# Performance work log

Hardware: AMD Instinct MI355X
Metric: run time of the kernel (lower is better)

Reference implementation:

```python
import jax, jax.numpy as jnp
import numpy as np

N, E = 100000, 1600000
IN_C, H, C = 256, 4, 64
NEG_SLOPE = 0.2


def setup_inputs() -> dict:
    key = jax.random.key(0)
    k1, k2, k3, k4, k5 = jax.random.split(key, 5)
    x = jax.random.normal(k1, (N, IN_C), dtype=jnp.float32)
    edge_index = jax.random.randint(k2, (2, E), 0, N, dtype=jnp.int64)
    # GATConv params: lin weight [IN_C, H*C], attention vectors [H, C], bias [C] (concat=False)
    W = jax.random.normal(k3, (IN_C, H * C), dtype=jnp.float32) / np.sqrt(IN_C)
    att_src = jax.random.normal(k4, (H, C), dtype=jnp.float32) / np.sqrt(C)
    att_dst = jax.random.normal(k5, (H, C), dtype=jnp.float32) / np.sqrt(C)
    bias = jnp.zeros((C,), dtype=jnp.float32)
    return {"x": x, "edge_index": edge_index, "W": W,
            "att_src": att_src, "att_dst": att_dst, "bias": bias}


def reference(x, edge_index, W, att_src, att_dst, bias):
    n = x.shape[0]
    # GATConv adds self-loops by default
    loops = jnp.arange(n, dtype=edge_index.dtype)
    src = jnp.concatenate([edge_index[0], loops])  # message source j
    dst = jnp.concatenate([edge_index[1], loops])  # message target i

    h = (x @ W).reshape(n, H, C)                       # [N,H,C]
    a_src = jnp.einsum('nhc,hc->nh', h, att_src)       # [N,H]
    a_dst = jnp.einsum('nhc,hc->nh', h, att_dst)       # [N,H]

    e = jax.nn.leaky_relu(a_src[src] + a_dst[dst], NEG_SLOPE)  # [E+N,H]
    m = jax.ops.segment_max(e, dst, num_segments=n)            # per-target max
    e = jnp.exp(e - m[dst])
    denom = jax.ops.segment_sum(e, dst, num_segments=n)
    alpha = e / (denom[dst] + 1e-16)                           # softmax over incoming edges

    out = jax.ops.segment_sum(alpha[:, :, None] * h[src], dst, num_segments=n)  # [N,H,C]
    return out.mean(axis=1) + bias  # concat=False -> mean over heads, [N,C]
```

## Files before the change

### kernel.cpp

```cpp
#include <hip/hip_runtime.h>

#define N_NODES 100000
#define N_EDGES 1600000
#define TOT (N_EDGES + N_NODES)
#define IN_CH 256
#define NHEAD 4
#define CH 64
#define HC 256
#define NEG_SLOPE 0.2f

typedef _Float16 half8 __attribute__((ext_vector_type(8)));
typedef _Float16 h2v __attribute__((ext_vector_type(2)));
typedef float f32x4 __attribute__((ext_vector_type(4)));
typedef unsigned short ushort_t;
typedef unsigned int uint_t;

static __device__ __forceinline__ ushort_t f2h(float f) {
  _Float16 h = (_Float16)f;
  return __builtin_bit_cast(ushort_t, h);
}

__global__ __launch_bounds__(256) void conv_w(const float* __restrict__ W,
                                              ushort_t* __restrict__ Wt) {
  int n = blockIdx.x * 4 + (threadIdx.x >> 6);
  int k0 = (threadIdx.x & 63) * 4;
  ushort4 u;
  u.x = f2h(W[(size_t)(k0 + 0) * HC + n]);
  u.y = f2h(W[(size_t)(k0 + 1) * HC + n]);
  u.z = f2h(W[(size_t)(k0 + 2) * HC + n]);
  u.w = f2h(W[(size_t)(k0 + 3) * HC + n]);
  *reinterpret_cast<ushort4*>(&Wt[(size_t)n * IN_CH + k0]) = u;
}

#define GBM 128
#define GBK 32
#define LDA 40

__global__ __launch_bounds__(256) void gemm_mfma(const float* __restrict__ X,
                                                 const ushort_t* __restrict__ Wt,
                                                 const float* __restrict__ att_src,
                                                 const float* __restrict__ att_dst,
                                                 uint2* __restrict__ Hmp,
                                                 float* __restrict__ as_out,
                                                 float* __restrict__ ad_out, int M) {
  __shared__ __align__(16) ushort_t As[GBM][LDA];
  __shared__ __align__(16) ushort_t Bs[HC][LDA];
  const int tid = threadIdx.x;
  const int lane = tid & 63;
  const int wid = tid >> 6;
  const int l16 = lane & 15;
  const int lhi = lane >> 4;
  const int row0 = blockIdx.x * GBM;

  f32x4 acc[2][16] = {};

  for (int k0 = 0; k0 < IN_CH; k0 += GBK) {
    {
      int r = tid >> 1;
      int c0 = (tid & 1) * 16;
      int gr = row0 + r;
      float4 v0, v1, v2, v3;
      if (gr < M) {
        const float4* p = reinterpret_cast<const float4*>(X + (size_t)gr * IN_CH + k0 + c0);
        v0 = p[0]; v1 = p[1]; v2 = p[2]; v3 = p[3];
      } else {
        v0 = v1 = v2 = v3 = make_float4(0.f, 0.f, 0.f, 0.f);
      }
      uint4 u0, u1;
      u0.x = __builtin_bit_cast(uint_t, __builtin_amdgcn_cvt_pkrtz(v0.x, v0.y));
      u0.y = __builtin_bit_cast(uint_t, __builtin_amdgcn_cvt_pkrtz(v0.z, v0.w));
      u0.z = __builtin_bit_cast(uint_t, __builtin_amdgcn_cvt_pkrtz(v1.x, v1.y));
      u0.w = __builtin_bit_cast(uint_t, __builtin_amdgcn_cvt_pkrtz(v1.z, v1.w));
      u1.x = __builtin_bit_cast(uint_t, __builtin_amdgcn_cvt_pkrtz(v2.x, v2.y));
      u1.y = __builtin_bit_cast(uint_t, __builtin_amdgcn_cvt_pkrtz(v2.z, v2.w));
      u1.z = __builtin_bit_cast(uint_t, __builtin_amdgcn_cvt_pkrtz(v3.x, v3.y));
      u1.w = __builtin_bit_cast(uint_t, __builtin_amdgcn_cvt_pkrtz(v3.z, v3.w));
      *reinterpret_cast<uint4*>(&As[r][c0]) = u0;
      *reinterpret_cast<uint4*>(&As[r][c0 + 8]) = u1;
    }
    {
      const uint4* p = reinterpret_cast<const uint4*>(Wt + (size_t)tid * IN_CH + k0);
      uint4 w0 = p[0], w1 = p[1];
      *reinterpret_cast<uint4*>(&Bs[tid][0]) = w0;
      *reinterpret_cast<uint4*>(&Bs[tid][8]) = w1;
      p = reinterpret_cast<const uint4*>(Wt + (size_t)tid * IN_CH + k0 + 16);
      uint4 w2 = p[0], w3 = p[1];
      *reinterpret_cast<uint4*>(&Bs[tid][16]) = w2;
      *reinterpret_cast<uint4*>(&Bs[tid][24]) = w3;
    }
    __syncthreads();
    half8 a0 = *reinterpret_cast<const half8*>(&As[wid * 32 + l16][lhi * 8]);
    half8 a1 = *reinterpret_cast<const half8*>(&As[wid * 32 + 16 + l16][lhi * 8]);
#pragma unroll
    for (int n = 0; n < 16; ++n) {
      half8 b = *reinterpret_cast<const half8*>(&Bs[n * 16 + l16][lhi * 8]);
      acc[0][n] = __builtin_amdgcn_mfma_f32_16x16x32_f16(a0, b, acc[0][n], 0, 0, 0);
      acc[1][n] = __builtin_amdgcn_mfma_f32_16x16x32_f16(a1, b, acc[1][n], 0, 0, 0);
    }
    __syncthreads();
  }

  float attS[16], attD[16];
#pragma unroll
  for (int n = 0; n < 16; ++n) {
    attS[n] = att_src[n * 16 + l16];
    attD[n] = att_dst[n * 16 + l16];
  }

#pragma unroll
  for (int m = 0; m < 2; ++m) {
#pragma unroll
    for (int r = 0; r < 4; ++r) {
      int grow = row0 + wid * 32 + m * 16 + lhi * 4 + r;
      if (grow < M) {
#pragma unroll
        for (int n2 = 0; n2 < 4; ++n2) {
          uint_t pk01 = __builtin_bit_cast(uint_t,
              __builtin_amdgcn_cvt_pkrtz(acc[m][n2][r], acc[m][n2 + 4][r]));
          uint_t pk23 = __builtin_bit_cast(uint_t,
              __builtin_amdgcn_cvt_pkrtz(acc[m][n2 + 8][r], acc[m][n2 + 12][r]));
          Hmp[(size_t)grow * 64 + n2 * 16 + l16] = make_uint2(pk01, pk23);
        }
        float s[4] = {0.f, 0.f, 0.f, 0.f}, d[4] = {0.f, 0.f, 0.f, 0.f};
#pragma unroll
        for (int h = 0; h < 4; ++h)
#pragma unroll
          for (int j = 0; j < 4; ++j) {
            s[h] += acc[m][h * 4 + j][r] * attS[h * 4 + j];
            d[h] += acc[m][h * 4 + j][r] * attD[h * 4 + j];
          }
#pragma unroll
        for (int off = 1; off < 16; off <<= 1)
#pragma unroll
          for (int h = 0; h < 4; ++h) {
            s[h] += __shfl_xor(s[h], off, 16);
            d[h] += __shfl_xor(d[h], off, 16);
          }
        if (l16 == 0) {
#pragma unroll
          for (int h = 0; h < 4; ++h) {
            as_out[(size_t)grow * 4 + h] = s[h];
            ad_out[(size_t)grow * 4 + h] = d[h];
          }
        }
      }
    }
  }
}

__global__ __launch_bounds__(256) void init_deg(int* __restrict__ deg) {
  int i = blockIdx.x * 256 + threadIdx.x;
  if (i < N_NODES) deg[i] = 1;
}

__global__ __launch_bounds__(256) void count_deg(const int* __restrict__ edst,
                                                 int* __restrict__ deg) {
  int t = blockIdx.x * 256 + threadIdx.x;
  if (t >= N_EDGES / 4) return;
  int4 d4 = reinterpret_cast<const int4*>(edst)[t];
  atomicAdd(&deg[d4.x], 1);
  atomicAdd(&deg[d4.y], 1);
  atomicAdd(&deg[d4.z], 1);
  atomicAdd(&deg[d4.w], 1);
}

__global__ __launch_bounds__(256) void scan1(const int* __restrict__ deg,
                                             int* __restrict__ rp,
                                             int* __restrict__ bsum) {
  __shared__ int sh[256];
  int t = threadIdx.x;
  int base = blockIdx.x * 1024 + t * 4;
  int v[4];
#pragma unroll
  for (int i = 0; i < 4; ++i) v[i] = (base + i < N_NODES) ? deg[base + i] : 0;
  int tsum = v[0] + v[1] + v[2] + v[3];
  sh[t] = tsum;
  __syncthreads();
  for (int off = 1; off < 256; off <<= 1) {
    int x = (t >= off) ? sh[t - off] : 0;
    __syncthreads();
    sh[t] += x;
    __syncthreads();
  }
  if (t == 255) bsum[blockIdx.x] = sh[255];
  int run = sh[t] - tsum;
#pragma unroll
  for (int i = 0; i < 4; ++i) {
    if (base + i < N_NODES) rp[base + i] = run;
    run += v[i];
  }
}

#define NBLK1 ((N_NODES + 1023) / 1024)

__global__ __launch_bounds__(128) void scan2(const int* __restrict__ bsum,
                                             int* __restrict__ boff) {
  __shared__ int sh[128];
  int t = threadIdx.x;
  int own = (t < NBLK1) ? bsum[t] : 0;
  sh[t] = own;
  __syncthreads();
  for (int off = 1; off < 128; off <<= 1) {
    int x = (t >= off) ? sh[t - off] : 0;
    __syncthreads();
    sh[t] += x;
    __syncthreads();
  }
  boff[t] = sh[t] - own;
}

__global__ __launch_bounds__(256) void scan3(int* __restrict__ rp,
                                             const int* __restrict__ boff,
                                             int* __restrict__ cursor) {
  int idx = blockIdx.x * 256 + threadIdx.x;
  if (idx < N_NODES) {
    int v = rp[idx] + boff[idx >> 10];
    rp[idx] = v;
    cursor[idx] = v;
  }
  if (idx == 0) rp[N_NODES] = TOT;
}

__global__ __launch_bounds__(256) void scatter_edges(const int* __restrict__ esrc,
                                                     const int* __restrict__ edst,
                                                     const float* __restrict__ as_buf,
                                                     const float* __restrict__ ad_buf,
                                                     int* __restrict__ cursor,
                                                     uint4* __restrict__ erec) {
  int e = blockIdx.x * 256 + threadIdx.x;
  if (e >= TOT) return;
  int s, d;
  if (e < N_EDGES) { s = esrc[e]; d = edst[e]; }
  else { s = e - N_EDGES; d = s; }
  int p = atomicAdd(&cursor[d], 1);
  float4 a1 = *reinterpret_cast<const float4*>(as_buf + (size_t)s * NHEAD);
  float4 a2 = *reinterpret_cast<const float4*>(ad_buf + (size_t)d * NHEAD);
  float e0 = a1.x + a2.x; e0 = e0 > 0.f ? e0 : NEG_SLOPE * e0;
  float e1 = a1.y + a2.y; e1 = e1 > 0.f ? e1 : NEG_SLOPE * e1;
  float e2 = a1.z + a2.z; e2 = e2 > 0.f ? e2 : NEG_SLOPE * e2;
  float e3 = a1.w + a2.w; e3 = e3 > 0.f ? e3 : NEG_SLOPE * e3;
  float w0 = __expf(e0 - 4.f), w1 = __expf(e1 - 4.f);
  float w2 = __expf(e2 - 4.f), w3 = __expf(e3 - 4.f);
  uint_t pk01 = __builtin_bit_cast(uint_t, __builtin_amdgcn_cvt_pkrtz(w0, w1));
  uint_t pk23 = __builtin_bit_cast(uint_t, __builtin_amdgcn_cvt_pkrtz(w2, w3));
  erec[p] = make_uint4((uint_t)s, pk01, pk23, 0u);
}

__global__ __launch_bounds__(256) void aggregate(const int* __restrict__ rp,
                                                 const uint4* __restrict__ erec,
                                                 const uint2* __restrict__ Hp,
                                                 const float* __restrict__ bias,
                                                 float* __restrict__ out) {
  int n = blockIdx.x * 4 + (threadIdx.x >> 6);
  int lane = threadIdx.x & 63;
  if (n >= N_NODES) return;
  const int half = lane >> 5;
  const uint_t off_lane = (uint_t)(lane & 31) << 4;
  const char* __restrict__ Hb = (const char*)Hp;

  int beg = rp[n], end = rp[n + 1];

  float acc[8] = {};
  float den[4] = {};

  int idx0 = beg + half; if (idx0 > end - 1) idx0 = end - 1;
  uint4 rec = erec[idx0];

  for (int j = beg; j < end; j += 2) {
    uint4 cur = rec;
    int idn = j + 2 + half; if (idn > end - 1) idn = end - 1;
    rec = erec[idn];

    bool act = (j + half) < end;
    uint_t w01u = act ? cur.y : 0u;
    uint_t w23u = act ? cur.z : 0u;

    uint_t hoff = (cur.x << 9) | off_lane;
    uint4 hv = *reinterpret_cast<const uint4*>(Hb + hoff);

    h2v w01 = __builtin_bit_cast(h2v, w01u);
    h2v w23 = __builtin_bit_cast(h2v, w23u);
    h2v ha = __builtin_bit_cast(h2v, hv.x);
    h2v hb = __builtin_bit_cast(h2v, hv.y);
    h2v hc = __builtin_bit_cast(h2v, hv.z);
    h2v hd = __builtin_bit_cast(h2v, hv.w);

    acc[0] += (float)w01.x * (float)ha.x;
    acc[1] += (float)w01.y * (float)ha.y;
    acc[2] += (float)w23.x * (float)hb.x;
    acc[3] += (float)w23.y * (float)hb.y;
    acc[4] += (float)w01.x * (float)hc.x;
    acc[5] += (float)w01.y * (float)hc.y;
    acc[6] += (float)w23.x * (float)hd.x;
    acc[7] += (float)w23.y * (float)hd.y;
    den[0] += (float)w01.x;
    den[1] += (float)w01.y;
    den[2] += (float)w23.x;
    den[3] += (float)w23.y;
  }

#pragma unroll
  for (int k = 0; k < 8; ++k) acc[k] += __shfl_xor(acc[k], 32, 64);
#pragma unroll
  for (int k = 0; k < 4; ++k) den[k] += __shfl_xor(den[k], 32, 64);

  if (lane < 32) {
    float i0 = 1.f / (den[0] + 1e-30f);
    float i1 = 1.f / (den[1] + 1e-30f);
    float i2 = 1.f / (den[2] + 1e-30f);
    float i3 = 1.f / (den[3] + 1e-30f);
    float2 b2 = *reinterpret_cast<const float2*>(bias + 2 * lane);
    float rA = 0.25f * (acc[0] * i0 + acc[1] * i1 + acc[2] * i2 + acc[3] * i3) + b2.x;
    float rB = 0.25f * (acc[4] * i0 + acc[5] * i1 + acc[6] * i2 + acc[7] * i3) + b2.y;
    *reinterpret_cast<float2*>(out + (size_t)n * CH + 2 * lane) = make_float2(rA, rB);
  }
}

extern "C" void kernel_launch(void* const* d_in, const int* in_sizes, int n_in,
                              void* d_out, int out_size, void* d_ws, size_t ws_size,
                              hipStream_t stream) {
  const float* x       = (const float*)d_in[0];
  const int*   eidx    = (const int*)d_in[1];
  const float* W       = (const float*)d_in[2];
  const float* att_src = (const float*)d_in[3];
  const float* att_dst = (const float*)d_in[4];
  const float* bias    = (const float*)d_in[5];
  float* out = (float*)d_out;

  uint2*    Hmp    = (uint2*)d_ws;
  uint4*    erec   = (uint4*)(Hmp + (size_t)N_NODES * 64);
  float*    as_buf = (float*)(erec + (size_t)TOT);
  float*    ad_buf = as_buf + (size_t)N_NODES * NHEAD;
  ushort_t* Wt     = (ushort_t*)(ad_buf + (size_t)N_NODES * NHEAD);
  int*      deg    = (int*)(Wt + 65536);
  int*      rp     = deg + N_NODES;
  int*      bsum   = rp + N_NODES + 1;
  int*      boff   = bsum + 128;

  const int* esrc = eidx;
  const int* edst = eidx + N_EDGES;

  conv_w<<<64, 256, 0, stream>>>(W, Wt);

  dim3 ggrid((N_NODES + GBM - 1) / GBM);
  gemm_mfma<<<ggrid, 256, 0, stream>>>(x, Wt, att_src, att_dst, Hmp, as_buf, ad_buf, N_NODES);

  init_deg<<<(N_NODES + 255) / 256, 256, 0, stream>>>(deg);
  count_deg<<<(N_EDGES / 4 + 255) / 256, 256, 0, stream>>>(edst, deg);
  scan1<<<NBLK1, 256, 0, stream>>>(deg, rp, bsum);
  scan2<<<1, 128, 0, stream>>>(bsum, boff);
  scan3<<<(N_NODES + 255) / 256, 256, 0, stream>>>(rp, boff, deg );
  scatter_edges<<<(TOT + 255) / 256, 256, 0, stream>>>(esrc, edst, as_buf, ad_buf,
                                                       deg , erec);

  aggregate<<<(N_NODES + 3) / 4, 256, 0, stream>>>(rp, erec, Hmp, bias, out);
}
```

Before: 354.2 us.

## Fuse degree counting into GEMM tail and unroll aggregate gather loop

The separate init_deg and count_deg kernels are removed. The degree array is now zeroed with a memset, and each GEMM block atomically counts a slice of destination indices after its tile finishes. scan1 adds 1 per node to account for self-loops. Separately, the aggregate loop now processes four edges per iteration, with two prefetched record streams and two outstanding H gathers, to expose more memory-level parallelism. The cost is extra register pressure in aggregate and atomic traffic appended to the GEMM kernel's tail.

```diff
diff --git a/kernel.cpp b/kernel.cpp
--- a/kernel.cpp
+++ b/kernel.cpp
@@ -42,7 +42,9 @@
                                                  const float* __restrict__ att_dst,
                                                  uint2* __restrict__ Hmp,
                                                  float* __restrict__ as_out,
-                                                 float* __restrict__ ad_out, int M) {
+                                                 float* __restrict__ ad_out,
+                                                 const int* __restrict__ edst,
+                                                 int* __restrict__ deg, int M) {
   __shared__ __align__(16) ushort_t As[GBM][LDA];
   __shared__ __align__(16) ushort_t Bs[HC][LDA];
   const int tid = threadIdx.x;
@@ -146,22 +148,18 @@
       }
     }
   }
-}
-
-__global__ __launch_bounds__(256) void init_deg(int* __restrict__ deg) {
-  int i = blockIdx.x * 256 + threadIdx.x;
-  if (i < N_NODES) deg[i] = 1;
-}
-
-__global__ __launch_bounds__(256) void count_deg(const int* __restrict__ edst,
-                                                 int* __restrict__ deg) {
-  int t = blockIdx.x * 256 + threadIdx.x;
-  if (t >= N_EDGES / 4) return;
-  int4 d4 = reinterpret_cast<const int4*>(edst)[t];
-  atomicAdd(&deg[d4.x], 1);
-  atomicAdd(&deg[d4.y], 1);
-  atomicAdd(&deg[d4.z], 1);
-  atomicAdd(&deg[d4.w], 1);
+
+#pragma unroll
+  for (int i = 0; i < 2; ++i) {
+    int t = blockIdx.x * 512 + i * 256 + tid;
+    if (t < N_EDGES / 4) {
+      int4 d4 = reinterpret_cast<const int4*>(edst)[t];
+      atomicAdd(&deg[d4.x], 1);
+      atomicAdd(&deg[d4.y], 1);
+      atomicAdd(&deg[d4.z], 1);
+      atomicAdd(&deg[d4.w], 1);
+    }
+  }
 }
 
 __global__ __launch_bounds__(256) void scan1(const int* __restrict__ deg,
@@ -172,7 +170,7 @@
   int base = blockIdx.x * 1024 + t * 4;
   int v[4];
 #pragma unroll
-  for (int i = 0; i < 4; ++i) v[i] = (base + i < N_NODES) ? deg[base + i] : 0;
+  for (int i = 0; i < 4; ++i) v[i] = (base + i < N_NODES) ? (deg[base + i] + 1) : 0;
   int tsum = v[0] + v[1] + v[2] + v[3];
   sh[t] = tsum;
   __syncthreads();
@@ -259,44 +257,76 @@
   const char* __restrict__ Hb = (const char*)Hp;
 
   int beg = rp[n], end = rp[n + 1];
+  const int last = end - 1;
 
   float acc[8] = {};
   float den[4] = {};
 
-  int idx0 = beg + half; if (idx0 > end - 1) idx0 = end - 1;
-  uint4 rec = erec[idx0];
-
-  for (int j = beg; j < end; j += 2) {
-    uint4 cur = rec;
-    int idn = j + 2 + half; if (idn > end - 1) idn = end - 1;
-    rec = erec[idn];
-
-    bool act = (j + half) < end;
-    uint_t w01u = act ? cur.y : 0u;
-    uint_t w23u = act ? cur.z : 0u;
-
-    uint_t hoff = (cur.x << 9) | off_lane;
-    uint4 hv = *reinterpret_cast<const uint4*>(Hb + hoff);
-
-    h2v w01 = __builtin_bit_cast(h2v, w01u);
-    h2v w23 = __builtin_bit_cast(h2v, w23u);
-    h2v ha = __builtin_bit_cast(h2v, hv.x);
-    h2v hb = __builtin_bit_cast(h2v, hv.y);
-    h2v hc = __builtin_bit_cast(h2v, hv.z);
-    h2v hd = __builtin_bit_cast(h2v, hv.w);
-
-    acc[0] += (float)w01.x * (float)ha.x;
-    acc[1] += (float)w01.y * (float)ha.y;
-    acc[2] += (float)w23.x * (float)hb.x;
-    acc[3] += (float)w23.y * (float)hb.y;
-    acc[4] += (float)w01.x * (float)hc.x;
-    acc[5] += (float)w01.y * (float)hc.y;
-    acc[6] += (float)w23.x * (float)hd.x;
-    acc[7] += (float)w23.y * (float)hd.y;
-    den[0] += (float)w01.x;
-    den[1] += (float)w01.y;
-    den[2] += (float)w23.x;
-    den[3] += (float)w23.y;
+  int ia = beg + half;     if (ia > last) ia = last;
+  int ib = beg + 2 + half; if (ib > last) ib = last;
+  uint4 rec_a = erec[ia];
+  uint4 rec_b = erec[ib];
+
+  for (int j = beg; j < end; j += 4) {
+    uint4 cur_a = rec_a;
+    uint4 cur_b = rec_b;
+    ia = j + 4 + half; if (ia > last) ia = last;
+    ib = j + 6 + half; if (ib > last) ib = last;
+    rec_a = erec[ia];
+    rec_b = erec[ib];
+
+    uint_t hoff_a = (cur_a.x << 9) | off_lane;
+    uint_t hoff_b = (cur_b.x << 9) | off_lane;
+    uint4 hva = *reinterpret_cast<const uint4*>(Hb + hoff_a);
+    uint4 hvb = *reinterpret_cast<const uint4*>(Hb + hoff_b);
+
+    bool act_a = (j + half) < end;
+    bool act_b = (j + 2 + half) < end;
+    uint_t wa01u = act_a ? cur_a.y : 0u;
+    uint_t wa23u = act_a ? cur_a.z : 0u;
+    uint_t wb01u = act_b ? cur_b.y : 0u;
+    uint_t wb23u = act_b ? cur_b.z : 0u;
+
+    h2v wa01 = __builtin_bit_cast(h2v, wa01u);
+    h2v wa23 = __builtin_bit_cast(h2v, wa23u);
+    h2v wb01 = __builtin_bit_cast(h2v, wb01u);
+    h2v wb23 = __builtin_bit_cast(h2v, wb23u);
+
+    h2v haa = __builtin_bit_cast(h2v, hva.x);
+    h2v hab = __builtin_bit_cast(h2v, hva.y);
+    h2v hac = __builtin_bit_cast(h2v, hva.z);
+    h2v had = __builtin_bit_cast(h2v, hva.w);
+
+    acc[0] += (float)wa01.x * (float)haa.x;
+    acc[1] += (float)wa01.y * (float)haa.y;
+    acc[2] += (float)wa23.x * (float)hab.x;
+    acc[3] += (float)wa23.y * (float)hab.y;
+    acc[4] += (float)wa01.x * (float)hac.x;
+    acc[5] += (float)wa01.y * (float)hac.y;
+    acc[6] += (float)wa23.x * (float)had.x;
+    acc[7] += (float)wa23.y * (float)had.y;
+    den[0] += (float)wa01.x;
+    den[1] += (float)wa01.y;
+    den[2] += (float)wa23.x;
+    den[3] += (float)wa23.y;
+
+    h2v hba = __builtin_bit_cast(h2v, hvb.x);
+    h2v hbb = __builtin_bit_cast(h2v, hvb.y);
+    h2v hbc = __builtin_bit_cast(h2v, hvb.z);
+    h2v hbd = __builtin_bit_cast(h2v, hvb.w);
+
+    acc[0] += (float)wb01.x * (float)hba.x;
+    acc[1] += (float)wb01.y * (float)hba.y;
+    acc[2] += (float)wb23.x * (float)hbb.x;
+    acc[3] += (float)wb23.y * (float)hbb.y;
+    acc[4] += (float)wb01.x * (float)hbc.x;
+    acc[5] += (float)wb01.y * (float)hbc.y;
+    acc[6] += (float)wb23.x * (float)hbd.x;
+    acc[7] += (float)wb23.y * (float)hbd.y;
+    den[0] += (float)wb01.x;
+    den[1] += (float)wb01.y;
+    den[2] += (float)wb23.x;
+    den[3] += (float)wb23.y;
   }
 
 #pragma unroll
@@ -341,12 +371,12 @@
   const int* edst = eidx + N_EDGES;
 
   conv_w<<<64, 256, 0, stream>>>(W, Wt);
+  hipMemsetAsync(deg, 0, (size_t)N_NODES * sizeof(int), stream);
 
   dim3 ggrid((N_NODES + GBM - 1) / GBM);
-  gemm_mfma<<<ggrid, 256, 0, stream>>>(x, Wt, att_src, att_dst, Hmp, as_buf, ad_buf, N_NODES);
-
-  init_deg<<<(N_NODES + 255) / 256, 256, 0, stream>>>(deg);
-  count_deg<<<(N_EDGES / 4 + 255) / 256, 256, 0, stream>>>(edst, deg);
+  gemm_mfma<<<ggrid, 256, 0, stream>>>(x, Wt, att_src, att_dst, Hmp, as_buf, ad_buf,
+                                       edst, deg, N_NODES);
+
   scan1<<<NBLK1, 256, 0, stream>>>(deg, rp, bsum);
   scan2<<<1, 128, 0, stream>>>(bsum, boff);
   scan3<<<(N_NODES + 255) / 256, 256, 0, stream>>>(rp, boff, deg );
```

Measured after the change: 338.4 us. 1.05x faster.
